# Kernel optimization log

Measured on AMD Instinct MI355X. Metric: run time of the kernel, lower is better.

The kernel has to match this reference:

```python
import jax, jax.numpy as jnp
import numpy as np

B, T, E = 2, 4096, 768
H, Dh = 12, 64
W = 256  # one-sided window
GLOBAL_IDX = np.arange(0, 4096, 256)  # 16 global token positions
G = GLOBAL_IDX.shape[0]
NEG = -1e9


def setup_inputs() -> dict:
    key = jax.random.key(0)
    ks = jax.random.split(key, 13)
    p = lambda k, shape: jax.random.normal(k, shape, dtype=jnp.float32) * 0.02
    inp = {"x": jax.random.normal(ks[0], (B, T, E), dtype=jnp.float32)}
    for n_i, n in enumerate(["q", "k", "v", "qg", "kg", "vg"]):
        inp["W" + n] = p(ks[1 + 2 * n_i], (E, E))
        inp["b" + n] = p(ks[2 + 2 * n_i], (E,))
    return inp


def _heads(t):
    # [B,T,E] -> [B,H,T,Dh]
    return t.reshape(B, -1, H, Dh).transpose(0, 2, 1, 3)


def _chunk(t, w):
    # [B,H,T,d] -> [B,H,nc,3w,d]: key/value chunks covering [c*w - w, c*w + 2w)
    nc = T // w
    tp = jnp.pad(t, ((0, 0), (0, 0), (w, w), (0, 0)))
    idx = jnp.arange(nc)[:, None] * w + jnp.arange(3 * w)[None, :]
    return tp[:, :, idx, :]


def _forward(x, Wq, bq, Wk, bk, Wv, bv, Wqg, bqg, Wkg, bkg, Wvg, bvg):
    scale = 1.0 / np.sqrt(Dh)
    q = _heads(x @ Wq + bq) * scale
    k = _heads(x @ Wk + bk)
    v = _heads(x @ Wv + bv)
    nc = T // W
    qc = q.reshape(B, H, nc, W, Dh)
    kc = _chunk(k, W)
    vc = _chunk(v, W)
    # banded local scores via 3-chunk trick: [B,H,nc,W,3W]
    scores = jnp.einsum('bhcid,bhcjd->bhcij', qc, kc)
    i = jnp.arange(W)
    j = jnp.arange(3 * W)
    band = (j[None, :] >= i[:, None]) & (j[None, :] <= i[:, None] + 2 * W)  # |diff|<=W
    key_pos = jnp.arange(nc)[:, None] * W + j[None, :] - W  # [nc,3W] absolute key pos
    inseq = (key_pos >= 0) & (key_pos < T)
    valid = band[None] & inseq[:, None, :]  # [nc,W,3W]
    # remove global tokens from windowed attention (float -10000 mask, HF-style)
    is_glob = jnp.zeros((T,), jnp.float32).at[jnp.asarray(GLOBAL_IDX)].set(1.0)
    gmask = is_glob[jnp.clip(key_pos, 0, T - 1)] * inseq
    scores = scores - 10000.0 * gmask[None, None, :, None, :]
    scores = jnp.where(valid[None, None], scores, NEG)
    # every query also attends to global keys (local k/v projections gathered)
    k_glob = k[:, :, GLOBAL_IDX, :]  # [B,H,G,Dh]
    v_glob = v[:, :, GLOBAL_IDX, :]
    gscores = jnp.einsum('bhcid,bhgd->bhcig', qc, k_glob)  # [B,H,nc,W,G]
    allp = jax.nn.softmax(jnp.concatenate([gscores, scores], axis=-1), axis=-1)
    pg = allp[..., :G]
    pl = allp[..., G:] * valid[None, None]
    out = (jnp.einsum('bhcij,bhcjd->bhcid', pl, vc)
           + jnp.einsum('bhcig,bhgd->bhcid', pg, v_glob))
    out = out.reshape(B, H, T, Dh).transpose(0, 2, 1, 3).reshape(B, T, E)
    # global-query tokens: full attention with global projections, overwrite rows
    xg = x[:, GLOBAL_IDX, :]  # [B,G,E]
    qg = (xg @ Wqg + bqg).reshape(B, G, H, Dh).transpose(0, 2, 1, 3) * scale
    kgl = _heads(x @ Wkg + bkg)
    vgl = _heads(x @ Wvg + bvg)
    gp = jax.nn.softmax(jnp.einsum('bhgd,bhtd->bhgt', qg, kgl), axis=-1)
    go = jnp.einsum('bhgt,bhtd->bhgd', gp, vgl).transpose(0, 2, 1, 3).reshape(B, G, E)
    return out.at[:, GLOBAL_IDX, :].set(go)


def reference(x, Wq, bq, Wk, bk, Wv, bv, Wqg, bqg, Wkg, bkg, Wvg, bvg):
    return _forward(x, Wq, bq, Wk, bk, Wv, bv, Wqg, bqg, Wkg, bkg, Wvg, bvg)
```

## Files before the change

### kernel.cpp

```cpp
#include <hip/hip_runtime.h>
#include <stdint.h>
#include <stddef.h>

#define BB 2
#define TT 4096
#define EE 768
#define HH 12
#define DH 64
#define WW 256
#define NCHUNK 16
#define GG 16

typedef __bf16 bf16_t;
typedef __bf16 bf16x8 __attribute__((ext_vector_type(8)));
typedef float f32x4 __attribute__((ext_vector_type(4)));

__device__ inline f32x4 mfma16(bf16x8 a, bf16x8 b, f32x4 c) {
    return __builtin_amdgcn_mfma_f32_16x16x32_bf16(a, b, c, 0, 0, 0);
}

__device__ inline void gload16(const void* g, void* l) {
    __builtin_amdgcn_global_load_lds(
        (const __attribute__((address_space(1))) void*)g,
        (__attribute__((address_space(3))) void*)l, 16, 0, 0);
}

__global__ __launch_bounds__(256) void k_prep(const float* __restrict__ x,
                                              bf16_t* __restrict__ xb,
                                              const float* __restrict__ w0,
                                              const float* __restrict__ w1,
                                              const float* __restrict__ w2,
                                              const float* __restrict__ w3,
                                              const float* __restrict__ w4,
                                              bf16_t* __restrict__ wt) {
    __shared__ __align__(16) bf16_t ls[64 * 65];
    const int tid = threadIdx.x;
    if (blockIdx.x < 3072) {
        const int i = (blockIdx.x * 256 + tid) * 8;
        f32x4 a = *(const f32x4*)(x + i);
        f32x4 b = *(const f32x4*)(x + i + 4);
        bf16x8 o;
        o[0] = (bf16_t)a[0]; o[1] = (bf16_t)a[1]; o[2] = (bf16_t)a[2]; o[3] = (bf16_t)a[3];
        o[4] = (bf16_t)b[0]; o[5] = (bf16_t)b[1]; o[6] = (bf16_t)b[2]; o[7] = (bf16_t)b[3];
        *(bf16x8*)(xb + i) = o;
    } else {
        const int idx0 = blockIdx.x - 3072;
        const int z = idx0 / 144;
        const int rr = idx0 % 144;
        const int k0 = (rr / 12) * 64;
        const int n0 = (rr % 12) * 64;
        const float* W = (z == 0) ? w0 : (z == 1) ? w1 : (z == 2) ? w2 : (z == 3) ? w3 : w4;
        #pragma unroll
        for (int i = 0; i < 16; ++i) {
            int idx = i * 256 + tid;
            int kr = idx >> 6, nc = idx & 63;
            ls[nc * 65 + kr] = (bf16_t)W[(size_t)(k0 + kr) * EE + n0 + nc];
        }
        __syncthreads();
        bf16_t* o = wt + (size_t)z * EE * EE;
        #pragma unroll
        for (int i = 0; i < 16; ++i) {
            int idx = i * 256 + tid;
            int nr = idx >> 6, kc = idx & 63;
            o[(size_t)(n0 + nr) * EE + k0 + kc] = ls[nr * 65 + kc];
        }
    }
}

__global__ __launch_bounds__(256) void k_gemm(const bf16_t* __restrict__ xb,
                                              const bf16_t* __restrict__ wt,
                                              const float* __restrict__ b0,
                                              const float* __restrict__ b1,
                                              const float* __restrict__ b2,
                                              const float* __restrict__ b3,
                                              const float* __restrict__ b4,
                                              bf16_t* __restrict__ proj,
                                              bf16_t* __restrict__ vTp) {
    const int tid = threadIdx.x;
    const int z = blockIdx.z;
    const int m0 = blockIdx.x * 128;
    const int n0 = blockIdx.y * 128;
    const float* bias = (z == 0) ? b0 : (z == 1) ? b1 : (z == 2) ? b2 : (z == 3) ? b3 : b4;
    const float scale = (z == 0) ? 0.125f : 1.0f;
    const bf16_t* wz = wt + (size_t)z * EE * EE;
    bf16_t* dst = proj + (size_t)z * BB * HH * TT * DH;

    __shared__ __align__(16) char smem[65536];
    bf16_t* ct = (bf16_t*)smem;

    const int lane = tid & 63, wid = tid >> 6;
    const int wr = wid >> 1, wc = wid & 1;
    const int lg = lane >> 4, lr = lane & 15;
    const int srow = lane >> 3;
    const int scol = (lane & 7) * 8;

    f32x4 acc[4][4];
    const f32x4 z4 = {0.f, 0.f, 0.f, 0.f};
    #pragma unroll
    for (int i = 0; i < 4; ++i)
        #pragma unroll
        for (int j = 0; j < 4; ++j) acc[i][j] = z4;

    #pragma unroll
    for (int i = 0; i < 4; ++i) {
        const int seg = wid * 4 + i;
        const int row = seg * 8 + srow;
        gload16(xb + (size_t)(m0 + row) * EE + scol, smem + seg * 1024);
        gload16(wz + (size_t)(n0 + row) * EE + scol, smem + 16384 + seg * 1024);
    }
    __syncthreads();

    for (int kt = 0; kt < 12; ++kt) {
        const int cur = kt & 1;
        bf16_t* lA = (bf16_t*)(smem + cur * 32768);
        bf16_t* lB = (bf16_t*)(smem + cur * 32768 + 16384);

        if (kt < 11) {
            const int k0 = (kt + 1) * 64;
            char* nb = smem + (cur ^ 1) * 32768;
            #pragma unroll
            for (int i = 0; i < 4; ++i) {
                const int seg = wid * 4 + i;
                const int row = seg * 8 + srow;
                gload16(xb + (size_t)(m0 + row) * EE + k0 + scol, nb + seg * 1024);
                gload16(wz + (size_t)(n0 + row) * EE + k0 + scol, nb + 16384 + seg * 1024);
            }
        }

        #pragma unroll
        for (int kk = 0; kk < 2; ++kk) {
            bf16x8 af[4], bfr[4];
            #pragma unroll
            for (int mi = 0; mi < 4; ++mi)
                af[mi] = *(const bf16x8*)(&lA[(wr * 64 + mi * 16 + lr) * 64 + kk * 32 + lg * 8]);
            #pragma unroll
            for (int ni = 0; ni < 4; ++ni)
                bfr[ni] = *(const bf16x8*)(&lB[(wc * 64 + ni * 16 + lr) * 64 + kk * 32 + lg * 8]);
            #pragma unroll
            for (int mi = 0; mi < 4; ++mi)
                #pragma unroll
                for (int ni = 0; ni < 4; ++ni)
                    acc[mi][ni] = mfma16(af[mi], bfr[ni], acc[mi][ni]);
        }
        __syncthreads();
    }

    #pragma unroll
    for (int mi = 0; mi < 4; ++mi)
        #pragma unroll
        for (int ni = 0; ni < 4; ++ni) {
            const int nl = wc * 64 + ni * 16 + lr;
            const float bn = bias[n0 + nl];
            #pragma unroll
            for (int r = 0; r < 4; ++r) {
                const int ml_ = wr * 64 + mi * 16 + lg * 4 + r;
                ct[ml_ * 128 + nl] = (bf16_t)((acc[mi][ni][r] + bn) * scale);
            }
        }
    __syncthreads();

    if (z != 2) {
        #pragma unroll
        for (int it = 0; it < 8; ++it) {
            const int idx = it * 2048 + tid * 8;
            const int row = idx >> 7, col = idx & 127;
            const int m = m0 + row, n = n0 + col;
            const int h = n >> 6, d = n & 63;
            const int bb = m >> 12, t = m & 4095;
            *(bf16x8*)(dst + (((size_t)bb * HH + h) * TT + t) * DH + d) = *(const bf16x8*)(&ct[idx]);
        }
    } else {
        const int bb = m0 >> 12, tbase = m0 & 4095;
        #pragma unroll
        for (int it = 0; it < 8; ++it) {
            const int idx = it * 2048 + tid * 8;
            const int nl = idx >> 7;
            const int tp0 = idx & 127;
            const int h = (n0 + nl) >> 6, d = (n0 + nl) & 63;
            bf16x8 v;
            #pragma unroll
            for (int j = 0; j < 8; ++j) {
                const int tpl = tp0 + j;
                const int tau = tpl >> 6, s = tpl & 63;
                const int tl = tau * 64 + (s & 3) * 16 + (s >> 2);
                v[j] = ct[tl * 128 + nl];
            }
            *(bf16x8*)(vTp + (((size_t)bb * HH + h) * DH + d) * TT + tbase + tp0) = v;
        }
    }
}

__global__ __launch_bounds__(256) void k_attn(const bf16_t* __restrict__ qs,
                                              const bf16_t* __restrict__ ks,
                                              const bf16_t* __restrict__ vT,
                                              const float* __restrict__ x,
                                              const float* __restrict__ Wqg,
                                              const float* __restrict__ bqg,
                                              const bf16_t* __restrict__ kgl,
                                              const bf16_t* __restrict__ vgl,
                                              float* __restrict__ out) {
    __shared__ __align__(16) char smem[26880];
    const int tid = threadIdx.x;

    if (blockIdx.x < 1536) {
        const int gx0 = blockIdx.x;
        const int gx = (gx0 & 7) * 192 + (gx0 >> 3);
        const int q4 = gx & 3;
        const int c = (gx >> 2) & 15;
        const int bh = gx >> 6;
        const int b = bh / HH, h = bh % HH;
        const int w = tid >> 6;
        const int parity = w & 1;
        const int qbase = (w >> 1) * 32;
        const int lane = tid & 63, lg = lane >> 4, lr = lane & 15;

        const bf16_t* qp = qs + ((size_t)bh * TT + c * WW + q4 * 64 + qbase) * DH;
        const bf16_t* kp = ks + (size_t)bh * TT * DH;
        const bf16_t* vp = vT + (size_t)bh * DH * TT;

        bf16_t* Pw  = (bf16_t*)(smem + (size_t)w * 4608);
        bf16_t* Kg  = (bf16_t*)(smem + 18432);
        bf16_t* VgT = (bf16_t*)(smem + 20736);
        float*  ml  = (float*)(smem + 25856);
        float*  OmP = (float*)(smem + (size_t)(w >> 1) * 8192);

        if (w == 0) {
            #pragma unroll
            for (int i = 0; i < 2; ++i) {
                int idx = i * 64 + lane;
                int r = idx >> 3, d8 = (idx & 7) * 8;
                *(bf16x8*)(&Kg[r * 72 + d8]) = *(const bf16x8*)(kp + (size_t)r * WW * DH + d8);
            }
        } else if (w == 1) {
            #pragma unroll
            for (int g = 0; g < 32; ++g)
                VgT[lane * 40 + g] = (g < 16) ? vp[(size_t)lane * TT + g * WW] : (bf16_t)0.f;
        }

        bf16x8 Qf[2][2];
        #pragma unroll
        for (int mi = 0; mi < 2; ++mi)
            #pragma unroll
            for (int kk = 0; kk < 2; ++kk)
                Qf[mi][kk] = *(const bf16x8*)(qp + (size_t)(mi * 16 + lr) * DH + kk * 32 + lg * 8);

        f32x4 O[2][4];
        const f32x4 z4 = {0.f, 0.f, 0.f, 0.f};
        #pragma unroll
        for (int i = 0; i < 2; ++i)
            #pragma unroll
            for (int j = 0; j < 4; ++j) O[i][j] = z4;

        float m_own[8], l_own[8];
        #pragma unroll
        for (int i = 0; i < 8; ++i) { m_own[i] = -1e30f; l_own[i] = 0.f; }

        __syncthreads();

        for (int ts = parity; ts < 10; ts += 2) {
            const bool isg = (ts == 0);
            const int jt = q4 + ts - 1;
            const int ttile = 4 * (c - 1) + jt;
            if (!isg && (ttile < 0 || ttile > 63)) continue;
            const bool gdrop = !isg && ((jt & 3) == 0);
            const bool anymask = (ts == 1) || (ts == 9) || gdrop;

            bf16x8 kf[4][2];
            if (isg) {
                #pragma unroll
                for (int kk = 0; kk < 2; ++kk)
                    kf[0][kk] = *(const bf16x8*)(&Kg[lr * 72 + kk * 32 + lg * 8]);
            } else {
                const bf16_t* ktp = kp + (size_t)ttile * 64 * DH;
                #pragma unroll
                for (int ni = 0; ni < 4; ++ni)
                    #pragma unroll
                    for (int kk = 0; kk < 2; ++kk)
                        kf[ni][kk] = *(const bf16x8*)(ktp + (size_t)(ni * 16 + lr) * DH + kk * 32 + lg * 8);
            }

            #pragma unroll
            for (int mi = 0; mi < 2; ++mi) {
                f32x4 S[4] = {z4, z4, z4, z4};
                if (isg) {
                    #pragma unroll
                    for (int kk = 0; kk < 2; ++kk)
                        S[0] = mfma16(Qf[mi][kk], kf[0][kk], S[0]);
                } else {
                    #pragma unroll
                    for (int kk = 0; kk < 2; ++kk)
                        #pragma unroll
                        for (int ni = 0; ni < 4; ++ni)
                            S[ni] = mfma16(Qf[mi][kk], kf[ni][kk], S[ni]);
                }

                #pragma unroll
                for (int r = 0; r < 4; ++r) {
                    const int lrow = mi * 16 + lg * 4 + r;
                    const int row = qbase + lrow;
                    const int idx = mi * 4 + r;
                    float sv[4];
                    if (anymask || isg) {
                        #pragma unroll
                        for (int ni = 0; ni < 4; ++ni) {
                            const int cc = ni * 16 + lr;
                            bool ok = isg ? (ni == 0)
                                          : !((ts == 1 && cc < row) || (ts == 9 && cc > row) ||
                                              (gdrop && cc == 0));
                            sv[ni] = ok ? S[ni][r] : -1e30f;
                        }
                    } else {
                        #pragma unroll
                        for (int ni = 0; ni < 4; ++ni) sv[ni] = S[ni][r];
                    }
                    const float town = fmaxf(fmaxf(sv[0], sv[1]), fmaxf(sv[2], sv[3]));
                    if (!__all(town <= m_own[idx] + 8.f)) {
                        float tmax = town;
                        tmax = fmaxf(tmax, __shfl_xor(tmax, 1));
                        tmax = fmaxf(tmax, __shfl_xor(tmax, 2));
                        tmax = fmaxf(tmax, __shfl_xor(tmax, 4));
                        tmax = fmaxf(tmax, __shfl_xor(tmax, 8));
                        const float m2 = fmaxf(m_own[idx], tmax);
                        const float scr = __expf(m_own[idx] - m2);
                        m_own[idx] = m2;
                        l_own[idx] *= scr;
                        #pragma unroll
                        for (int di = 0; di < 4; ++di) O[mi][di][r] *= scr;
                    }
                    const float p0 = __expf(sv[0] - m_own[idx]);
                    const float p1 = __expf(sv[1] - m_own[idx]);
                    const float p2 = __expf(sv[2] - m_own[idx]);
                    const float p3 = __expf(sv[3] - m_own[idx]);
                    l_own[idx] += (p0 + p1) + (p2 + p3);
                    if (isg) {
                        Pw[lrow * 72 + 0 * 16 + lr] = (bf16_t)p0;
                        Pw[lrow * 72 + 1 * 16 + lr] = (bf16_t)p1;
                        Pw[lrow * 72 + 2 * 16 + lr] = (bf16_t)p2;
                        Pw[lrow * 72 + 3 * 16 + lr] = (bf16_t)p3;
                    } else {
                        uint32_t d0, d1;
                        asm("v_cvt_pk_bf16_f32 %0, %1, %2" : "=v"(d0) : "v"(p0), "v"(p1));
                        asm("v_cvt_pk_bf16_f32 %0, %1, %2" : "=v"(d1) : "v"(p2), "v"(p3));
                        uint32_t* dstp = (uint32_t*)(&Pw[lrow * 72 + lr * 4]);
                        dstp[0] = d0;
                        dstp[1] = d1;
                    }
                }
            }

            asm volatile("s_waitcnt lgkmcnt(0)" ::: "memory");
            __builtin_amdgcn_sched_barrier(0);

            #pragma unroll
            for (int kkp = 0; kkp < 2; ++kkp) {
                if (isg && kkp == 1) continue;
                bf16x8 pa[2];
                #pragma unroll
                for (int mi = 0; mi < 2; ++mi)
                    pa[mi] = *(const bf16x8*)(&Pw[(mi * 16 + lr) * 72 + kkp * 32 + lg * 8]);
                #pragma unroll
                for (int di = 0; di < 4; ++di) {
                    bf16x8 vf;
                    if (isg)
                        vf = *(const bf16x8*)(&VgT[(di * 16 + lr) * 40 + lg * 8]);
                    else
                        vf = *(const bf16x8*)(vp + (size_t)(di * 16 + lr) * TT + ttile * 64 + kkp * 32 + lg * 8);
                    #pragma unroll
                    for (int mi = 0; mi < 2; ++mi) O[mi][di] = mfma16(pa[mi], vf, O[mi][di]);
                }
            }
        }

        #pragma unroll
        for (int i = 0; i < 8; ++i) {
            float l = l_own[i];
            l += __shfl_xor(l, 1);
            l += __shfl_xor(l, 2);
            l += __shfl_xor(l, 4);
            l += __shfl_xor(l, 8);
            l_own[i] = l;
        }

        #pragma unroll
        for (int mi = 0; mi < 2; ++mi)
            #pragma unroll
            for (int r = 0; r < 4; ++r)
                if (lr == 0) {
                    int lrow = mi * 16 + lg * 4 + r;
                    ml[w * 64 + lrow]      = m_own[mi * 4 + r];
                    ml[w * 64 + 32 + lrow] = l_own[mi * 4 + r];
                }
        __syncthreads();

        if (parity) {
            #pragma unroll
            for (int mi = 0; mi < 2; ++mi)
                #pragma unroll
                for (int r = 0; r < 4; ++r) {
                    const int lrow = mi * 16 + lg * 4 + r;
                    const int idx = mi * 4 + r;
                    const float mstar = fmaxf(ml[(w - 1) * 64 + lrow], m_own[idx]);
                    const float s1 = __expf(m_own[idx] - mstar);
                    #pragma unroll
                    for (int di = 0; di < 4; ++di)
                        OmP[lrow * 64 + di * 16 + lr] = O[mi][di][r] * s1;
                    if (lr == 0) ml[w * 64 + 32 + lrow] = l_own[idx] * s1;
                }
        }
        __syncthreads();

        if (!parity) {
            const bool gskip = (q4 == 0) && (qbase == 0);
            const size_t outbase = ((size_t)b * TT + c * WW + q4 * 64 + qbase) * EE + h * DH;
            #pragma unroll
            for (int mi = 0; mi < 2; ++mi)
                #pragma unroll
                for (int r = 0; r < 4; ++r) {
                    const int lrow = mi * 16 + lg * 4 + r;
                    const int idx = mi * 4 + r;
                    const float m1 = ml[(w + 1) * 64 + lrow];
                    const float mstar = fmaxf(m_own[idx], m1);
                    const float s0 = __expf(m_own[idx] - mstar);
                    const float l = l_own[idx] * s0 + ml[(w + 1) * 64 + 32 + lrow];
                    const float linv = 1.f / l;
                    if (gskip && lrow == 0) continue;
                    #pragma unroll
                    for (int di = 0; di < 4; ++di)
                        out[outbase + (size_t)lrow * EE + di * 16 + lr] =
                            (O[mi][di][r] * s0 + OmP[lrow * 64 + di * 16 + lr]) * linv;
                }
        }
    } else {
        const int gx0 = blockIdx.x - 1536;
        const int xcd = gx0 & 7, y = gx0 >> 3;
        const int bh = xcd * 3 + (y >> 4);
        const int g = y & 15;
        const int b = bh / HH, h = bh % HH;
        const int lane = tid & 63, w = tid >> 6;

        float* qrow = (float*)smem;
        float* sc   = (float*)(smem + 256);
        float* red  = (float*)(smem + 16640);
        float* xr   = (float*)(smem + 17664);

        const float* xrow = x + ((size_t)b * TT + g * WW) * EE;
        for (int i = tid; i < EE; i += 256) xr[i] = xrow[i];
        __syncthreads();
        {
            const int d = tid & 63;
            const int e0 = (tid >> 6) * 192;
            float p = 0.f;
            for (int e = e0; e < e0 + 192; ++e)
                p += xr[e] * Wqg[(size_t)e * EE + h * DH + d];
            red[tid] = p;
        }
        __syncthreads();
        if (tid < DH)
            qrow[tid] = (red[tid] + red[64 + tid] + red[128 + tid] + red[192 + tid]
                         + bqg[h * DH + tid]) * 0.125f;
        __syncthreads();

        const bf16_t* kp = kgl + (size_t)bh * TT * DH;
        float lmax = -1e30f;
        for (int t = tid; t < TT; t += 256) {
            const bf16_t* kr = kp + (size_t)t * DH;
            float s = 0.f;
            #pragma unroll
            for (int d0 = 0; d0 < DH; d0 += 8) {
                bf16x8 kv = *(const bf16x8*)(kr + d0);
                #pragma unroll
                for (int jj = 0; jj < 8; ++jj) s += qrow[d0 + jj] * (float)kv[jj];
            }
            sc[t] = s;
            lmax = fmaxf(lmax, s);
        }
        #pragma unroll
        for (int off = 32; off; off >>= 1) lmax = fmaxf(lmax, __shfl_xor(lmax, off));
        if (lane == 0) red[w] = lmax;
        __syncthreads();
        const float M = fmaxf(fmaxf(red[0], red[1]), fmaxf(red[2], red[3]));
        float lsum = 0.f;
        for (int t = tid; t < TT; t += 256) {
            float p = __expf(sc[t] - M);
            sc[t] = p;
            lsum += p;
        }
        #pragma unroll
        for (int off = 32; off; off >>= 1) lsum += __shfl_xor(lsum, off);
        __syncthreads();
        if (lane == 0) red[64 + w] = lsum;
        __syncthreads();
        const float SUM = red[64] + red[65] + red[66] + red[67];
        __syncthreads();

        const bf16_t* vp = vgl + (size_t)bh * TT * DH;
        float a0 = 0.f, a1 = 0.f, a2 = 0.f, a3 = 0.f;
        const int tbase = w * 1024;
        for (int t = tbase; t < tbase + 1024; t += 4) {
            a0 += sc[t] * (float)vp[(size_t)t * DH + lane];
            a1 += sc[t + 1] * (float)vp[(size_t)(t + 1) * DH + lane];
            a2 += sc[t + 2] * (float)vp[(size_t)(t + 2) * DH + lane];
            a3 += sc[t + 3] * (float)vp[(size_t)(t + 3) * DH + lane];
        }
        red[tid] = (a0 + a1) + (a2 + a3);
        __syncthreads();
        if (w == 0) {
            float tot = red[lane] + red[64 + lane] + red[128 + lane] + red[192 + lane];
            out[((size_t)b * TT + g * WW) * EE + h * DH + lane] = tot / SUM;
        }
    }
}

extern "C" void kernel_launch(void* const* d_in, const int* in_sizes, int n_in,
                              void* d_out, int out_size, void* d_ws, size_t ws_size,
                              hipStream_t stream) {
    const float* x   = (const float*)d_in[0];
    const float* Wq  = (const float*)d_in[1];
    const float* bq  = (const float*)d_in[2];
    const float* Wk  = (const float*)d_in[3];
    const float* bk  = (const float*)d_in[4];
    const float* Wv  = (const float*)d_in[5];
    const float* bv  = (const float*)d_in[6];
    const float* Wqg = (const float*)d_in[7];
    const float* bqg = (const float*)d_in[8];
    const float* Wkg = (const float*)d_in[9];
    const float* bkg = (const float*)d_in[10];
    const float* Wvg = (const float*)d_in[11];
    const float* bvg = (const float*)d_in[12];
    float* out = (float*)d_out;

    const size_t NX = (size_t)BB * TT * EE;
    const size_t NW = (size_t)EE * EE;
    const size_t NP = (size_t)BB * HH * TT * DH;

    bf16_t* xb   = (bf16_t*)d_ws;
    bf16_t* wt   = xb + NX;
    bf16_t* proj = wt + 5 * NW;
    bf16_t* vT   = proj + 5 * NP;

    (void)bvg; (void)in_sizes; (void)n_in; (void)out_size; (void)ws_size;

    k_prep<<<dim3(3792), 256, 0, stream>>>(x, xb, Wq, Wk, Wv, Wkg, Wvg, wt);
    k_gemm<<<dim3(64, 6, 5), 256, 0, stream>>>(xb, wt, bq, bk, bv, bkg, bvg, proj, vT);
    k_attn<<<dim3(1920), 256, 0, stream>>>(proj, proj + NP, vT, x, Wqg, bqg,
                                           proj + 3 * NP, proj + 4 * NP, out);
}
```

Measured before the change: 223.7 us.

## Schedule global-query blocks first and vectorize their dot-product loops

```diff
diff --git a/kernel.cpp b/kernel.cpp
--- a/kernel.cpp
+++ b/kernel.cpp
@@ -202,8 +202,8 @@
     __shared__ __align__(16) char smem[26880];
     const int tid = threadIdx.x;
 
-    if (blockIdx.x < 1536) {
-        const int gx0 = blockIdx.x;
+    if (blockIdx.x >= 384) {
+        const int gx0 = blockIdx.x - 384;
         const int gx = (gx0 & 7) * 192 + (gx0 >> 3);
         const int q4 = gx & 3;
         const int c = (gx >> 2) & 15;
@@ -431,7 +431,7 @@
                 }
         }
     } else {
-        const int gx0 = blockIdx.x - 1536;
+        const int gx0 = blockIdx.x;
         const int xcd = gx0 & 7, y = gx0 >> 3;
         const int bh = xcd * 3 + (y >> 4);
         const int g = y & 15;
@@ -450,8 +450,13 @@
             const int d = tid & 63;
             const int e0 = (tid >> 6) * 192;
             float p = 0.f;
-            for (int e = e0; e < e0 + 192; ++e)
-                p += xr[e] * Wqg[(size_t)e * EE + h * DH + d];
+            for (int e = e0; e < e0 + 192; e += 4) {
+                f32x4 xv = *(const f32x4*)&xr[e];
+                p += xv[0] * Wqg[(size_t)e * EE + h * DH + d]
+                   + xv[1] * Wqg[(size_t)(e + 1) * EE + h * DH + d]
+                   + xv[2] * Wqg[(size_t)(e + 2) * EE + h * DH + d]
+                   + xv[3] * Wqg[(size_t)(e + 3) * EE + h * DH + d];
+            }
             red[tid] = p;
         }
         __syncthreads();
@@ -461,28 +466,35 @@
         __syncthreads();
 
         const bf16_t* kp = kgl + (size_t)bh * TT * DH;
+        float s_acc[16];
+        #pragma unroll
+        for (int i = 0; i < 16; ++i) s_acc[i] = 0.f;
+        #pragma unroll
+        for (int d0 = 0; d0 < DH; d0 += 8) {
+            const f32x4 qa = *(const f32x4*)&qrow[d0];
+            const f32x4 qb = *(const f32x4*)&qrow[d0 + 4];
+            #pragma unroll
+            for (int i = 0; i < 16; ++i) {
+                bf16x8 kv = *(const bf16x8*)(kp + (size_t)(tid + 256 * i) * DH + d0);
+                s_acc[i] += qa[0] * (float)kv[0] + qa[1] * (float)kv[1]
+                          + qa[2] * (float)kv[2] + qa[3] * (float)kv[3]
+                          + qb[0] * (float)kv[4] + qb[1] * (float)kv[5]
+                          + qb[2] * (float)kv[6] + qb[3] * (float)kv[7];
+            }
+        }
         float lmax = -1e30f;
-        for (int t = tid; t < TT; t += 256) {
-            const bf16_t* kr = kp + (size_t)t * DH;
-            float s = 0.f;
-            #pragma unroll
-            for (int d0 = 0; d0 < DH; d0 += 8) {
-                bf16x8 kv = *(const bf16x8*)(kr + d0);
-                #pragma unroll
-                for (int jj = 0; jj < 8; ++jj) s += qrow[d0 + jj] * (float)kv[jj];
-            }
-            sc[t] = s;
-            lmax = fmaxf(lmax, s);
-        }
+        #pragma unroll
+        for (int i = 0; i < 16; ++i) lmax = fmaxf(lmax, s_acc[i]);
         #pragma unroll
         for (int off = 32; off; off >>= 1) lmax = fmaxf(lmax, __shfl_xor(lmax, off));
         if (lane == 0) red[w] = lmax;
         __syncthreads();
         const float M = fmaxf(fmaxf(red[0], red[1]), fmaxf(red[2], red[3]));
         float lsum = 0.f;
-        for (int t = tid; t < TT; t += 256) {
-            float p = __expf(sc[t] - M);
-            sc[t] = p;
+        #pragma unroll
+        for (int i = 0; i < 16; ++i) {
+            float p = __expf(s_acc[i] - M);
+            sc[tid + 256 * i] = p;
             lsum += p;
         }
         #pragma unroll
@@ -494,15 +506,23 @@
         __syncthreads();
 
         const bf16_t* vp = vgl + (size_t)bh * TT * DH;
-        float a0 = 0.f, a1 = 0.f, a2 = 0.f, a3 = 0.f;
+        float a[8];
+        #pragma unroll
+        for (int i = 0; i < 8; ++i) a[i] = 0.f;
         const int tbase = w * 1024;
-        for (int t = tbase; t < tbase + 1024; t += 4) {
-            a0 += sc[t] * (float)vp[(size_t)t * DH + lane];
-            a1 += sc[t + 1] * (float)vp[(size_t)(t + 1) * DH + lane];
-            a2 += sc[t + 2] * (float)vp[(size_t)(t + 2) * DH + lane];
-            a3 += sc[t + 3] * (float)vp[(size_t)(t + 3) * DH + lane];
-        }
-        red[tid] = (a0 + a1) + (a2 + a3);
+        for (int t = tbase; t < tbase + 1024; t += 8) {
+            const f32x4 s0 = *(const f32x4*)&sc[t];
+            const f32x4 s1 = *(const f32x4*)&sc[t + 4];
+            a[0] += s0[0] * (float)vp[(size_t)(t + 0) * DH + lane];
+            a[1] += s0[1] * (float)vp[(size_t)(t + 1) * DH + lane];
+            a[2] += s0[2] * (float)vp[(size_t)(t + 2) * DH + lane];
+            a[3] += s0[3] * (float)vp[(size_t)(t + 3) * DH + lane];
+            a[4] += s1[0] * (float)vp[(size_t)(t + 4) * DH + lane];
+            a[5] += s1[1] * (float)vp[(size_t)(t + 5) * DH + lane];
+            a[6] += s1[2] * (float)vp[(size_t)(t + 6) * DH + lane];
+            a[7] += s1[3] * (float)vp[(size_t)(t + 7) * DH + lane];
+        }
+        red[tid] = ((a[0] + a[1]) + (a[2] + a[3])) + ((a[4] + a[5]) + (a[6] + a[7]));
         __syncthreads();
         if (w == 0) {
             float tot = red[lane] + red[64 + lane] + red[128 + lane] + red[192 + lane];
```

Measured after the change: 238.1 us. +6.4%, slower.
